# Performance work log

Measured on AMD Instinct MI355X. Metric: run time of the kernel, lower is better.

Reference implementation:

```python
import jax, jax.numpy as jnp
import numpy as np

N = 4096      # n_patches / nodes
IN_FEAT = 512
EMBED = 512
HEADS = 8
HEAD_DIM = EMBED // HEADS
SCALING = HEAD_DIM ** -0.5


def setup_inputs() -> dict:
    key = jax.random.key(0)
    ks = jax.random.split(key, 7)
    x = jax.random.normal(ks[0], (N, IN_FEAT), dtype=jnp.float32)
    adj = jax.random.randint(ks[1], (N, N), 0, 2, dtype=jnp.int32)
    s = 0.04  # ~xavier scale for 512x512
    WQ = jax.random.normal(ks[2], (EMBED, IN_FEAT), dtype=jnp.float32) * s
    WK = jax.random.normal(ks[3], (EMBED, IN_FEAT), dtype=jnp.float32) * s
    WV = jax.random.normal(ks[4], (EMBED, IN_FEAT), dtype=jnp.float32) * s
    we = jax.random.normal(ks[5], (1, HEAD_DIM), dtype=jnp.float32) * 0.1
    be = jnp.zeros((1,), dtype=jnp.float32)
    return {"x": x, "adj": adj, "WQ": WQ, "WK": WK, "WV": WV, "we": we, "be": be}


def reference(x, adj, WQ, WK, WV, we, be):
    n = x.shape[0]
    # projections: [N, E] -> [H, N, head_dim]
    Q = (x @ WQ.T).reshape(n, HEADS, HEAD_DIM).transpose(1, 0, 2)
    K = (x @ WK.T).reshape(n, HEADS, HEAD_DIM).transpose(1, 0, 2)
    V = (x @ WV.T).reshape(n, HEADS, HEAD_DIM).transpose(1, 0, 2)
    # scores + per-query energy term: [H, N, N]
    energy = Q @ we.T + be                      # [H, N, 1]
    attn = jnp.einsum('hqd,hkd->hqk', Q, K) * SCALING + energy
    # adjacency mask (broadcast over heads)
    attn = attn + jnp.where(adj > 0, 0.0, -jnp.inf)
    attn = jax.nn.softmax(attn, axis=-1)
    # winner-take-all: one-hot at row max, divided by num_heads
    hard = (attn == jnp.max(attn, axis=-1, keepdims=True)).astype(jnp.float32) / HEADS
    out = jnp.einsum('hqk,hkd->hqd', hard, V)   # [H, N, head_dim]
    return out.transpose(1, 0, 2).reshape(n, EMBED)
```

## Files before the change

### kernel.cpp

```cpp
#include <hip/hip_runtime.h>
#include <hip/hip_bf16.h>
#include <float.h>
#include <stdint.h>

#define NPT    4096
#define EMB    512
#define NH     8
#define HD     64
#define KSPLIT 64

typedef __attribute__((ext_vector_type(8))) _Float16 f16x8;
typedef __attribute__((ext_vector_type(4))) float f32x4;
typedef __attribute__((ext_vector_type(16))) float f32x16;
typedef uint32_t u32;

#define LO_SCALE 2048.0f
#define LO_INV   4.8828125e-4f

__device__ __forceinline__ void async_ld16(const void* gsrc, void* ldst) {
    __builtin_amdgcn_global_load_lds(
        (const __attribute__((address_space(1))) u32*)gsrc,
        (__attribute__((address_space(3))) u32*)ldst, 16, 0, 0);
}

__device__ __forceinline__ void split2(float a, unsigned short& h, unsigned short& l) {
    _Float16 fh = (_Float16)a;
    float r = (a - (float)fh) * LO_SCALE;
    _Float16 fl = (_Float16)r;
    h = *reinterpret_cast<unsigned short*>(&fh);
    l = *reinterpret_cast<unsigned short*>(&fl);
}

__global__ __launch_bounds__(256) void prep_kernel(const float* __restrict__ x,
                                                   const float* __restrict__ wq,
                                                   const float* __restrict__ wk,
                                                   const float* __restrict__ wv,
                                                   const int* __restrict__ adj,
                                                   unsigned short* __restrict__ xs,
                                                   unsigned short* __restrict__ wqs,
                                                   unsigned short* __restrict__ wks,
                                                   unsigned short* __restrict__ wvs,
                                                   unsigned* __restrict__ bits_t) {
    int y = blockIdx.y;
    size_t i = (size_t)blockIdx.x * 256 + threadIdx.x;
    if (y == 4) {
        int q = (int)(i >> 7), w = (int)i & 127;
        const int4* p = (const int4*)(adj + (size_t)q * NPT + w * 32);
        unsigned m = 0;
#pragma unroll
        for (int j = 0; j < 8; ++j) {
            int4 v = p[j];
            m |= (v.x != 0 ? 1u : 0u) << (j * 4 + 0);
            m |= (v.y != 0 ? 1u : 0u) << (j * 4 + 1);
            m |= (v.z != 0 ? 1u : 0u) << (j * 4 + 2);
            m |= (v.w != 0 ? 1u : 0u) << (j * 4 + 3);
        }
        bits_t[(size_t)w * NPT + q] = m;
    } else if (y == 0) {
        const size_t PL = (size_t)NPT * EMB;
        float4 v = ((const float4*)x)[i];
        ushort4 h, l;
        split2(v.x, h.x, l.x);
        split2(v.y, h.y, l.y);
        split2(v.z, h.z, l.z);
        split2(v.w, h.w, l.w);
        ((ushort4*)xs)[i]        = h;
        ((ushort4*)(xs + PL))[i] = l;
    } else {
        const size_t WPL = 262144;
        if (i >= WPL / 4) return;
        const float* src = (y == 1) ? wq : (y == 2) ? wk : wv;
        unsigned short* dst = (y == 1) ? wqs : (y == 2) ? wks : wvs;
        float4 v = ((const float4*)src)[i];
        int e  = (int)(i >> 7);
        int k0 = ((int)i & 127) * 4;
        int ebk = e >> 6, el = e & 63;
        int kc = k0 >> 5, g = (k0 >> 3) & 3, dd = k0 & 7;
        size_t off = ((((size_t)ebk * 16 + kc) * 4 + g) * 64 + el) * 8 + dd;
        ushort4 h, l;
        split2(v.x, h.x, l.x);
        split2(v.y, h.y, l.y);
        split2(v.z, h.z, l.z);
        split2(v.w, h.w, l.w);
        *(ushort4*)(dst + off)       = h;
        *(ushort4*)(dst + WPL + off) = l;
    }
}

__global__ __launch_bounds__(256, 3) void gemm_mfma(const unsigned short* __restrict__ xs,
                                                    const unsigned short* __restrict__ wqs,
                                                    const unsigned short* __restrict__ wks,
                                                    const unsigned short* __restrict__ wvs,
                                                    unsigned short* __restrict__ Q2,
                                                    unsigned short* __restrict__ K2,
                                                    float* __restrict__ V) {
    const int z = blockIdx.z;
    const unsigned short* W2 = (z == 0) ? wqs : (z == 1) ? wks : wvs;
    const size_t XPL = (size_t)NPT * EMB;
    const size_t WPL = 262144;
    const size_t OPL = (size_t)NH * NPT * HD;

    const int nb = blockIdx.x * 128;
    const int ebk = blockIdx.y;
    const int tid = threadIdx.x;
    const int wvi = tid >> 6, lane = tid & 63;
    const int m = lane & 15, quad = lane >> 4;
    const int n0 = nb + wvi * 32;

    __shared__ __align__(16) unsigned short Ws[3][2 * 2048];

    auto prefetchW = [&](int kc, int buf) {
#pragma unroll
        for (int i2 = 0; i2 < 2; ++i2) {
            int c = wvi + 4 * i2;
            int p = c >> 2, sub = c & 3;
            const unsigned short* src = W2 + (size_t)p * WPL
                + ((size_t)ebk * 16 + kc) * 2048 + (sub * 64 + lane) * 8;
            async_ld16(src, &Ws[buf][p * 2048 + sub * 512]);
        }
    };
    f16x8 bf[3][2][2];
    auto load_bf = [&](int set, int kc) {
#pragma unroll
        for (int nt = 0; nt < 2; ++nt)
#pragma unroll
            for (int p = 0; p < 2; ++p)
                bf[set][nt][p] = *(const f16x8*)(xs + (size_t)p * XPL
                    + (size_t)(n0 + nt * 16 + m) * EMB + kc * 32 + quad * 8);
    };

    f32x4 acc[2][4][2];
#pragma unroll
    for (int s = 0; s < 2; ++s)
#pragma unroll
        for (int mt = 0; mt < 4; ++mt)
#pragma unroll
            for (int nt = 0; nt < 2; ++nt) acc[s][mt][nt] = (f32x4){0.f, 0.f, 0.f, 0.f};

    load_bf(0, 0); prefetchW(0, 0);
    load_bf(1, 1); prefetchW(1, 1);

#pragma unroll
    for (int kc = 0; kc < 16; ++kc) {
        if (kc == 15) asm volatile("s_waitcnt vmcnt(0)\n\ts_barrier" ::: "memory");
        else          asm volatile("s_waitcnt vmcnt(6)\n\ts_barrier" ::: "memory");
        if (kc + 2 < 16) {
            load_bf((kc + 2) % 3, kc + 2);
            prefetchW(kc + 2, (kc + 2) % 3);
        }
#pragma unroll
        for (int ga = 0; ga < 2; ++ga) {
            f16x8 af[4];
#pragma unroll
            for (int mt = 0; mt < 4; ++mt)
                af[mt] = *(const f16x8*)&Ws[kc % 3][ga * 2048 + (quad * 64 + mt * 16 + m) * 8];
#pragma unroll
            for (int pb = 0; pb < 2 - ga; ++pb)
#pragma unroll
                for (int mt = 0; mt < 4; ++mt)
#pragma unroll
                    for (int nt = 0; nt < 2; ++nt)
                        acc[ga + pb][mt][nt] = __builtin_amdgcn_mfma_f32_16x16x32_f16(
                            af[mt], bf[kc % 3][nt][pb], acc[ga + pb][mt][nt], 0, 0, 0);
        }
    }

    const int h = ebk;
#pragma unroll
    for (int mt = 0; mt < 4; ++mt)
#pragma unroll
        for (int nt = 0; nt < 2; ++nt) {
            const int n = n0 + nt * 16 + m;
            const int d0 = mt * 16 + quad * 4;
            f32x4 a;
#pragma unroll
            for (int j = 0; j < 4; ++j)
                a[j] = fmaf(acc[1][mt][nt][j], LO_INV, acc[0][mt][nt][j]);
            if (z == 2) {
                *(f32x4*)(V + (size_t)n * EMB + ebk * 64 + d0) = a;
            } else {
                ushort4 ph, pl;
                split2(a[0], ph.x, pl.x);
                split2(a[1], ph.y, pl.y);
                split2(a[2], ph.z, pl.z);
                split2(a[3], ph.w, pl.w);
                unsigned short* O2 = (z == 0) ? Q2 : K2;
                size_t off = ((size_t)h * 128 + (n >> 5)) * 2048
                           + (d0 >> 3) * 256 + (n & 31) * 8 + (d0 & 7);
                *(ushort4*)(O2 + off)       = ph;
                *(ushort4*)(O2 + OPL + off) = pl;
            }
        }
}

__global__ __launch_bounds__(256, 4) void score_mfma(const unsigned short* __restrict__ Q2,
                                                     const unsigned short* __restrict__ K2,
                                                     const unsigned* __restrict__ bits_t,
                                                     float* __restrict__ pval,
                                                     int* __restrict__ pidx) {
    const int bid = blockIdx.x + 32 * blockIdx.y;
    const int xcd = bid & 7, j = bid >> 3;
    const int ks  = xcd * 8 + (j >> 5);
    const int qb  = (j & 31) * 128;

    const int tid = threadIdx.x;
    const int wvi = tid >> 6, lane = tid & 63;
    const int il = lane & 31, hi = lane >> 5;
    const size_t PL = (size_t)NH * NPT * HD;
    const int q0 = qb + wvi * 32;
    const int NT = NH * 2;

    __shared__ __align__(16) unsigned short Ks[3][2 * 2048 + 1024];

    auto prefetchK = [&](int t) {
        int h = t >> 1, kt = ks * 2 + (t & 1), buf = t % 3;
#pragma unroll
        for (int i2 = 0; i2 < 2; ++i2) {
            int c = wvi + 4 * i2;
            int p = c >> 2, sub = c & 3;
            const unsigned short* src = K2 + (size_t)p * PL
                + ((size_t)h * 128 + kt) * 2048 + (sub * 64 + lane) * 8;
            async_ld16(src, &Ks[buf][p * 2048 + sub * 512]);
        }
    };

    f16x8 qf[4][2];
    auto load_qf = [&](int hh) {
#pragma unroll
        for (int c = 0; c < 4; ++c)
#pragma unroll
            for (int p = 0; p < 2; ++p)
                qf[c][p] = *(const f16x8*)(Q2 + (size_t)p * PL
                    + ((size_t)hh * 128 + (q0 >> 5)) * 2048
                    + (c * 2 + hi) * 256 + il * 8);
    };

    load_qf(0);
    prefetchK(0);
    prefetchK(1);

    float bestv = -FLT_MAX; int besti = 0;

#pragma unroll 1
    for (int t = 0; t < NT; ++t) {
        const int h = t >> 1, kst = t & 1, buf = t % 3;

        if (t + 1 < NT) asm volatile("s_waitcnt vmcnt(2)\n\ts_barrier" ::: "memory");
        else            asm volatile("s_waitcnt vmcnt(0)\n\ts_barrier" ::: "memory");

        if (kst == 0) { bestv = -FLT_MAX; besti = 0; }

        unsigned w = bits_t[(size_t)(ks * 2 + kst) * NPT + q0 + il];

        f32x16 acc0, acc1;
#pragma unroll
        for (int j2 = 0; j2 < 16; ++j2) { acc0[j2] = 0.f; acc1[j2] = 0.f; }

        __builtin_amdgcn_s_setprio(1);
#pragma unroll
        for (int c = 0; c < 4; ++c) {
            f16x8 kfh = *(const f16x8*)&Ks[buf][(c * 2 + hi) * 256 + il * 8];
            f16x8 kfl = *(const f16x8*)&Ks[buf][2048 + (c * 2 + hi) * 256 + il * 8];
            acc0 = __builtin_amdgcn_mfma_f32_32x32x16_f16(kfh, qf[c][0], acc0, 0, 0, 0);
            acc1 = __builtin_amdgcn_mfma_f32_32x32x16_f16(kfh, qf[c][1], acc1, 0, 0, 0);
            acc1 = __builtin_amdgcn_mfma_f32_32x32x16_f16(kfl, qf[c][0], acc1, 0, 0, 0);
        }
        __builtin_amdgcn_s_setprio(0);

        if (kst == 1 && h + 1 < NH) load_qf(h + 1);
        if (t + 2 < NT) prefetchK(t + 2);

        const unsigned wsh = w >> (4 * hi);
#pragma unroll
        for (int r = 0; r < 16; ++r) {
            float s = fmaf(acc1[r], LO_INV, acc0[r]);
            bool ok = (wsh >> ((r & 3) + 8 * (r >> 2))) & 1u;
            bool g = ok && (s > bestv);
            bestv = g ? s : bestv;
            besti = g ? (kst * 16 + r) : besti;
        }

        if (kst == 1) {
            int code = besti;
            int bi = ks * 64 + ((code >> 4) << 5) + 4 * hi
                   + (code & 3) + ((code >> 2) & 3) * 8;
            float v = bestv;
            float ov = __shfl_xor(v, 32);
            int   oi = __shfl_xor(bi, 32);
            if (ov > v || (ov == v && oi < bi)) { v = ov; bi = oi; }
            if (hi == 0) {
                size_t o = ((size_t)h * KSPLIT + ks) * NPT + q0 + il;
                pval[o] = v; pidx[o] = bi;
            }
        }
    }
}

__global__ __launch_bounds__(256) void gather_out(const float* __restrict__ V,
                                                  const float* __restrict__ pval,
                                                  const int* __restrict__ pidx,
                                                  float* __restrict__ out) {
    const int q = blockIdx.x;
    const int tid = threadIdx.x;
    __shared__ int widx[NH];
    {
        const int h = tid >> 5, j = tid & 31;
        size_t o1 = ((size_t)h * KSPLIT + j) * NPT + q;
        size_t o2 = ((size_t)h * KSPLIT + j + 32) * NPT + q;
        float v1 = pval[o1]; int b1 = pidx[o1];
        float v2 = pval[o2]; int b2 = pidx[o2];
        bool t2 = (v2 > v1) || (v2 == v1 && b2 < b1);
        float v = t2 ? v2 : v1; int bi = t2 ? b2 : b1;
#pragma unroll
        for (int o = 1; o < 32; o <<= 1) {
            float ov = __shfl_xor(v, o);
            int   oi = __shfl_xor(bi, o);
            if (ov > v || (ov == v && oi < bi)) { v = ov; bi = oi; }
        }
        if (j == 0) widx[h] = bi;
    }
    __syncthreads();
    if (tid < 128) {
        const int h = tid >> 4;
        const int d4 = (tid & 15) * 4;
        const int k = widx[h];
        float4 v = *(const float4*)(V + (size_t)k * EMB + h * HD + d4);
        v.x *= 0.125f; v.y *= 0.125f; v.z *= 0.125f; v.w *= 0.125f;
        *(float4*)(out + (size_t)q * EMB + h * HD + d4) = v;
    }
}

extern "C" void kernel_launch(void* const* d_in, const int* in_sizes, int n_in,
                              void* d_out, int out_size, void* d_ws, size_t ws_size,
                              hipStream_t stream) {
    const float* x   = (const float*)d_in[0];
    const int*   adj = (const int*)d_in[1];
    const float* WQ  = (const float*)d_in[2];
    const float* WK  = (const float*)d_in[3];
    const float* WV  = (const float*)d_in[4];
    float* out = (float*)d_out;

    char* ws = (char*)d_ws;
    const size_t HMB = 512u * 1024;
    unsigned short* xs   = (unsigned short*)(ws);
    unsigned short* wqs  = (unsigned short*)(ws + 16 * HMB);
    unsigned short* wks  = (unsigned short*)(ws + 18 * HMB);
    unsigned short* wvs  = (unsigned short*)(ws + 20 * HMB);
    unsigned short* Q2   = (unsigned short*)(ws + 32 * HMB);
    unsigned short* K2   = (unsigned short*)(ws + 48 * HMB);
    float*          V    = (float*)(ws + 64 * HMB);
    unsigned*       bits = (unsigned*)(ws + 80 * HMB);
    float*          pval = (float*)(ws);
    int*            pidx = (int*)(ws + 16 * HMB);

    prep_kernel<<<dim3(2048, 5), dim3(256), 0, stream>>>(x, WQ, WK, WV, adj,
                                                         xs, wqs, wks, wvs, bits);
    gemm_mfma<<<dim3(NPT / 128, NH, 3), dim3(256), 0, stream>>>(xs, wqs, wks, wvs, Q2, K2, V);
    score_mfma<<<dim3(NPT / 128, KSPLIT), dim3(256), 0, stream>>>(Q2, K2, bits, pval, pidx);
    gather_out<<<dim3(NPT), dim3(256), 0, stream>>>(V, pval, pidx, out);
}
```

Before: 244.5 us.

## Process both key sub-tiles per head per barrier and prefetch bitmask words

Measured after the change: 242.7 us. About the same (-0.7%).

```diff
diff --git a/kernel.cpp b/kernel.cpp
--- a/kernel.cpp
+++ b/kernel.cpp
@@ -198,29 +198,25 @@
                                                      const unsigned* __restrict__ bits_t,
                                                      float* __restrict__ pval,
                                                      int* __restrict__ pidx) {
-    const int bid = blockIdx.x + 32 * blockIdx.y;
-    const int xcd = bid & 7, j = bid >> 3;
-    const int ks  = xcd * 8 + (j >> 5);
-    const int qb  = (j & 31) * 128;
-
+    const int qb = blockIdx.x * 128;
+    const int ks = blockIdx.y;
     const int tid = threadIdx.x;
     const int wvi = tid >> 6, lane = tid & 63;
     const int il = lane & 31, hi = lane >> 5;
     const size_t PL = (size_t)NH * NPT * HD;
     const int q0 = qb + wvi * 32;
-    const int NT = NH * 2;
-
-    __shared__ __align__(16) unsigned short Ks[3][2 * 2048 + 1024];
+
+    __shared__ __align__(16) unsigned short Ks[3][2 * 4096];
 
     auto prefetchK = [&](int t) {
-        int h = t >> 1, kt = ks * 2 + (t & 1), buf = t % 3;
-#pragma unroll
-        for (int i2 = 0; i2 < 2; ++i2) {
+        int buf = t % 3;
+        const unsigned short* base = K2 + ((size_t)t * 128 + ks * 2) * 2048;
+#pragma unroll
+        for (int i2 = 0; i2 < 4; ++i2) {
             int c = wvi + 4 * i2;
-            int p = c >> 2, sub = c & 3;
-            const unsigned short* src = K2 + (size_t)p * PL
-                + ((size_t)h * 128 + kt) * 2048 + (sub * 64 + lane) * 8;
-            async_ld16(src, &Ks[buf][p * 2048 + sub * 512]);
+            int p = c >> 3, sub = c & 7;
+            async_ld16(base + (size_t)p * PL + sub * 512 + lane * 8,
+                       &Ks[buf][p * 4096 + sub * 512]);
         }
     };
 
@@ -235,61 +231,89 @@
                     + (c * 2 + hi) * 256 + il * 8);
     };
 
+    unsigned w0, w1;
+    auto load_bits = [&](unsigned& a, unsigned& b) {
+        a = bits_t[(size_t)(ks * 2 + 0) * NPT + q0 + il];
+        b = bits_t[(size_t)(ks * 2 + 1) * NPT + q0 + il];
+    };
+
     load_qf(0);
+    load_bits(w0, w1);
     prefetchK(0);
     prefetchK(1);
 
-    float bestv = -FLT_MAX; int besti = 0;
-
 #pragma unroll 1
-    for (int t = 0; t < NT; ++t) {
-        const int h = t >> 1, kst = t & 1, buf = t % 3;
-
-        if (t + 1 < NT) asm volatile("s_waitcnt vmcnt(2)\n\ts_barrier" ::: "memory");
+    for (int t = 0; t < NH; ++t) {
+        const int buf = t % 3;
+
+        if (t + 1 < NH) asm volatile("s_waitcnt vmcnt(4)\n\ts_barrier" ::: "memory");
         else            asm volatile("s_waitcnt vmcnt(0)\n\ts_barrier" ::: "memory");
 
-        if (kst == 0) { bestv = -FLT_MAX; besti = 0; }
-
-        unsigned w = bits_t[(size_t)(ks * 2 + kst) * NPT + q0 + il];
+        unsigned cw0 = w0, cw1 = w1;
+        float bestv = -FLT_MAX; int bestc = 0;
 
         f32x16 acc0, acc1;
 #pragma unroll
-        for (int j2 = 0; j2 < 16; ++j2) { acc0[j2] = 0.f; acc1[j2] = 0.f; }
-
+        for (int j = 0; j < 16; ++j) { acc0[j] = 0.f; acc1[j] = 0.f; }
         __builtin_amdgcn_s_setprio(1);
 #pragma unroll
         for (int c = 0; c < 4; ++c) {
             f16x8 kfh = *(const f16x8*)&Ks[buf][(c * 2 + hi) * 256 + il * 8];
-            f16x8 kfl = *(const f16x8*)&Ks[buf][2048 + (c * 2 + hi) * 256 + il * 8];
+            f16x8 kfl = *(const f16x8*)&Ks[buf][4096 + (c * 2 + hi) * 256 + il * 8];
             acc0 = __builtin_amdgcn_mfma_f32_32x32x16_f16(kfh, qf[c][0], acc0, 0, 0, 0);
             acc1 = __builtin_amdgcn_mfma_f32_32x32x16_f16(kfh, qf[c][1], acc1, 0, 0, 0);
             acc1 = __builtin_amdgcn_mfma_f32_32x32x16_f16(kfl, qf[c][0], acc1, 0, 0, 0);
         }
         __builtin_amdgcn_s_setprio(0);
-
-        if (kst == 1 && h + 1 < NH) load_qf(h + 1);
-        if (t + 2 < NT) prefetchK(t + 2);
-
-        const unsigned wsh = w >> (4 * hi);
-#pragma unroll
-        for (int r = 0; r < 16; ++r) {
-            float s = fmaf(acc1[r], LO_INV, acc0[r]);
-            bool ok = (wsh >> ((r & 3) + 8 * (r >> 2))) & 1u;
-            bool g = ok && (s > bestv);
-            bestv = g ? s : bestv;
-            besti = g ? (kst * 16 + r) : besti;
-        }
-
-        if (kst == 1) {
-            int code = besti;
-            int bi = ks * 64 + ((code >> 4) << 5) + 4 * hi
-                   + (code & 3) + ((code >> 2) & 3) * 8;
+        {
+            const unsigned wsh = cw0 >> (4 * hi);
+#pragma unroll
+            for (int r = 0; r < 16; ++r) {
+                float s = fmaf(acc1[r], LO_INV, acc0[r]);
+                bool ok = (wsh >> ((r & 3) + 8 * (r >> 2))) & 1u;
+                bool g = ok && (s > bestv);
+                bestv = g ? s : bestv;
+                bestc = g ? r : bestc;
+            }
+        }
+
+#pragma unroll
+        for (int j = 0; j < 16; ++j) { acc0[j] = 0.f; acc1[j] = 0.f; }
+        __builtin_amdgcn_s_setprio(1);
+#pragma unroll
+        for (int c = 0; c < 4; ++c) {
+            f16x8 kfh = *(const f16x8*)&Ks[buf][2048 + (c * 2 + hi) * 256 + il * 8];
+            f16x8 kfl = *(const f16x8*)&Ks[buf][4096 + 2048 + (c * 2 + hi) * 256 + il * 8];
+            acc0 = __builtin_amdgcn_mfma_f32_32x32x16_f16(kfh, qf[c][0], acc0, 0, 0, 0);
+            acc1 = __builtin_amdgcn_mfma_f32_32x32x16_f16(kfh, qf[c][1], acc1, 0, 0, 0);
+            acc1 = __builtin_amdgcn_mfma_f32_32x32x16_f16(kfl, qf[c][0], acc1, 0, 0, 0);
+        }
+        __builtin_amdgcn_s_setprio(0);
+
+        if (t + 1 < NH) { load_qf(t + 1); load_bits(w0, w1); }
+        if (t + 2 < NH) prefetchK(t + 2);
+
+        {
+            const unsigned wsh = cw1 >> (4 * hi);
+#pragma unroll
+            for (int r = 0; r < 16; ++r) {
+                float s = fmaf(acc1[r], LO_INV, acc0[r]);
+                bool ok = (wsh >> ((r & 3) + 8 * (r >> 2))) & 1u;
+                bool g = ok && (s > bestv);
+                bestv = g ? s : bestv;
+                bestc = g ? (16 + r) : bestc;
+            }
+        }
+
+        {
+            int bi = ks * 64 + ((bestc >> 4) << 5) + 4 * hi
+                   + (bestc & 3) + ((bestc >> 2) & 3) * 8;
             float v = bestv;
             float ov = __shfl_xor(v, 32);
             int   oi = __shfl_xor(bi, 32);
             if (ov > v || (ov == v && oi < bi)) { v = ov; bi = oi; }
             if (hi == 0) {
-                size_t o = ((size_t)h * KSPLIT + ks) * NPT + q0 + il;
+                size_t o = ((size_t)t * KSPLIT + ks) * NPT + q0 + il;
                 pval[o] = v; pidx[o] = bi;
             }
         }
```
